# Optimization experiments

Hardware: AMD Instinct MI355X
Metric: run time of the kernel (lower is better)

Reference implementation:

```python
import jax, jax.numpy as jnp
import numpy as np

TOP_K = 2
NUM_EXPERTS = 8
ROUTE_SCALE = 1.0


def setup_inputs() -> dict:
    key = jax.random.key(0)
    ks = jax.random.split(key, 8)
    bs, slen, dim, hidden, E = 4, 1024, 2048, 1024, NUM_EXPERTS
    s = 0.02
    return {
        "x": jax.random.normal(ks[0], (bs, slen, dim), jnp.float32),
        "gate_w": jax.random.normal(ks[1], (E, dim), jnp.float32) * s,
        "w1": jax.random.normal(ks[2], (E, hidden, dim), jnp.float32) * s,
        "w2": jax.random.normal(ks[3], (E, dim, hidden), jnp.float32) * s,
        "w3": jax.random.normal(ks[4], (E, hidden, dim), jnp.float32) * s,
        "ws1": jax.random.normal(ks[5], (hidden, dim), jnp.float32) * s,
        "ws2": jax.random.normal(ks[6], (dim, hidden), jnp.float32) * s,
        "ws3": jax.random.normal(ks[7], (hidden, dim), jnp.float32) * s,
    }


def reference(x, gate_w, w1, w2, w3, ws1, ws2, ws3):
    bs, slen, dim = x.shape
    xf = x.reshape(-1, dim)  # (T, dim)
    # --- router: sigmoid scores in fp32, top-k (expert_bias is zeros at init) ---
    logits = (xf @ gate_w.T).astype(jnp.float32)  # (T, E)
    scores = jax.nn.sigmoid(logits)
    top_scores, sel_idx = jax.lax.top_k(scores, TOP_K)  # (T, k), (T, k)
    top_scores = top_scores * ROUTE_SCALE  # route_norm=False
    # --- routed experts: score_before_experts=True -> scale input by score ---
    routed = jnp.zeros_like(xf)
    for k in range(TOP_K):
        xs = xf * top_scores[:, k][:, None]  # (T, dim)
        h1 = jnp.einsum('td,ehd->teh', xs, w1)
        h3 = jnp.einsum('td,ehd->teh', xs, w3)
        h = jax.nn.silu(h1) * h3  # (T, E, hidden)
        onehot = jax.nn.one_hot(sel_idx[:, k], NUM_EXPERTS, dtype=h.dtype)  # (T, E)
        routed = routed + jnp.einsum('teh,te,edh->td', h, onehot, w2)
    # --- shared expert (SwiGLU FFN) ---
    shared = (jax.nn.silu(xf @ ws1.T) * (xf @ ws3.T)) @ ws2.T
    out = (shared + routed).reshape(bs, slen, dim)
    return out
```

## Files before the change

### kernel.cpp

```cpp
#include <hip/hip_runtime.h>
#include <hip/hip_bf16.h>
#include <cstdint>

#define TTOK   4096
#define DIM    2048
#define HID    1024
#define NEXP   8
#define GROWS  12288

typedef __attribute__((ext_vector_type(8))) __bf16 bf16x8;
typedef __attribute__((ext_vector_type(4))) float  f32x4;

__device__ __forceinline__ void glds16(const void* g, void* l) {
  __builtin_amdgcn_global_load_lds((const __attribute__((address_space(1))) void*)g,
                                   (__attribute__((address_space(3))) void*)l,
                                   16, 0, 0);
}

#define BAR() do { asm volatile("" ::: "memory"); __builtin_amdgcn_s_barrier(); \
                   asm volatile("" ::: "memory"); } while (0)

__global__ void convert_router_k(const float* __restrict__ w1, const float* __restrict__ w2,
                                 const float* __restrict__ w3, const float* __restrict__ ws1,
                                 const float* __restrict__ ws2, const float* __restrict__ ws3,
                                 __bf16* __restrict__ w13, __bf16* __restrict__ w2c,
                                 const float* __restrict__ x, const float* __restrict__ gw,
                                 int* __restrict__ sel, float* __restrict__ sco,
                                 int* __restrict__ counts) {
  const int N1 = 9 * 2048 * 2048 / 8;
  const int N2 = 9 * 2048 * 1024 / 8;
  const int CONV_BLOCKS = (N1 + N2) / 256;

  if (blockIdx.x < (unsigned)CONV_BLOCKS) {
    int s = blockIdx.x * 256 + threadIdx.x;
    const float* src;
    __bf16* dst;
    if (s < N1) {
      int e  = s / 524288;
      int r  = (s % 524288) / 256;
      int c  = (s % 256) * 8;
      int nr;
      if (r < 1024) { src = (e < 8 ? w1 + ((size_t)e * 1024 + r) * 2048 : ws1 + (size_t)r * 2048) + c;
                      nr = 2 * r; }
      else          { src = (e < 8 ? w3 + ((size_t)e * 1024 + (r - 1024)) * 2048 : ws3 + (size_t)(r - 1024) * 2048) + c;
                      nr = 2 * (r - 1024) + 1; }
      dst = w13 + ((size_t)e * 2048 + nr) * 2048 + c;
    } else {
      int s2 = s - N1;
      int e  = s2 / 262144;
      int r  = (s2 % 262144) / 128;
      int c  = (s2 % 128) * 8;
      src = (e < 8 ? w2 + ((size_t)e * 2048 + r) * 1024 : ws2 + (size_t)r * 1024) + c;
      dst = w2c + ((size_t)e * 2048 + r) * 1024 + c;
    }
    float4 a = *(const float4*)(src);
    float4 b = *(const float4*)(src + 4);
    bf16x8 o;
    o[0]=(__bf16)a.x; o[1]=(__bf16)a.y; o[2]=(__bf16)a.z; o[3]=(__bf16)a.w;
    o[4]=(__bf16)b.x; o[5]=(__bf16)b.y; o[6]=(__bf16)b.z; o[7]=(__bf16)b.w;
    *(bf16x8*)dst = o;
    return;
  }

  int t    = (blockIdx.x - CONV_BLOCKS) * 4 + (threadIdx.x >> 6);
  int lane = threadIdx.x & 63;
  const float* xr = x + (size_t)t * DIM;
  float acc[NEXP];
  #pragma unroll
  for (int e = 0; e < NEXP; ++e) acc[e] = 0.f;
  for (int d = lane * 4; d < DIM; d += 256) {
    float4 xv = *(const float4*)(xr + d);
    #pragma unroll
    for (int e = 0; e < NEXP; ++e) {
      float4 gv = *(const float4*)(gw + (size_t)e * DIM + d);
      acc[e] += xv.x * gv.x + xv.y * gv.y + xv.z * gv.z + xv.w * gv.w;
    }
  }
  #pragma unroll
  for (int off = 32; off; off >>= 1)
    #pragma unroll
    for (int e = 0; e < NEXP; ++e) acc[e] += __shfl_xor(acc[e], off);
  if (lane == 0) {
    float s[NEXP];
    #pragma unroll
    for (int e = 0; e < NEXP; ++e) s[e] = 1.f / (1.f + expf(-acc[e]));
    int e0 = 0;
    #pragma unroll
    for (int e = 1; e < NEXP; ++e) if (s[e] > s[e0]) e0 = e;
    int e1 = (e0 == 0) ? 1 : 0;
    #pragma unroll
    for (int e = 0; e < NEXP; ++e) if (e != e0 && s[e] > s[e1]) e1 = e;
    sel[2 * t] = e0; sel[2 * t + 1] = e1;
    sco[2 * t] = s[e0]; sco[2 * t + 1] = s[e1];
    atomicAdd(&counts[e0], 1); atomicAdd(&counts[e1], 1);
  }
}

__global__ void scan_k(const int* __restrict__ counts, int* __restrict__ offs) {
  if (threadIdx.x == 0 && blockIdx.x == 0) {
    int o = 0;
    for (int e = 0; e < NEXP; ++e) { offs[e] = o; o += counts[e]; }
    offs[NEXP] = o;
    offs[NEXP + 1] = o + TTOK;
  }
}

__global__ void gather_k(const float* __restrict__ x, const int* __restrict__ sel,
                         const float* __restrict__ sco, const int* __restrict__ offs,
                         int* __restrict__ cursor, int* __restrict__ token_rows,
                         __bf16* __restrict__ xg) {
  __shared__ int   rows[3];
  __shared__ float ss[3];
  int t = blockIdx.x;
  if (threadIdx.x == 0) {
    int e0 = sel[2 * t], e1 = sel[2 * t + 1];
    int r0 = offs[e0] + atomicAdd(&cursor[e0], 1);
    int r1 = offs[e1] + atomicAdd(&cursor[e1], 1);
    int r2 = 8192 + t;
    rows[0] = r0; rows[1] = r1; rows[2] = r2;
    ss[0] = sco[2 * t]; ss[1] = sco[2 * t + 1]; ss[2] = 1.0f;
    token_rows[3 * t] = r0; token_rows[3 * t + 1] = r1; token_rows[3 * t + 2] = r2;
  }
  __syncthreads();
  int c = threadIdx.x * 8;
  float4 v0 = *(const float4*)(x + (size_t)t * DIM + c);
  float4 v1 = *(const float4*)(x + (size_t)t * DIM + c + 4);
  #pragma unroll
  for (int j = 0; j < 3; ++j) {
    float s = ss[j];
    bf16x8 o;
    o[0]=(__bf16)(v0.x*s); o[1]=(__bf16)(v0.y*s); o[2]=(__bf16)(v0.z*s); o[3]=(__bf16)(v0.w*s);
    o[4]=(__bf16)(v1.x*s); o[5]=(__bf16)(v1.y*s); o[6]=(__bf16)(v1.z*s); o[7]=(__bf16)(v1.w*s);
    *(bf16x8*)(xg + (size_t)rows[j] * DIM + c) = o;
  }
}

template <int EPI>
__launch_bounds__(256)
__global__ void gemm_nt(const __bf16* __restrict__ A, const __bf16* __restrict__ Bw,
                        __bf16* __restrict__ Hb, float* __restrict__ c2a, float* __restrict__ c2b,
                        const int* __restrict__ offs, int K_, int N_) {
  int z  = blockIdx.z;
  int o0 = offs[z];
  int ne = offs[z + 1] - o0;

  int flat = blockIdx.y * 32 + blockIdx.x;
  int xcd  = flat & 7;
  int r    = flat >> 3;
  int s    = r >> 4;
  int pos  = r & 15;
  int bm   = ((xcd >> 2) + 2 * s) * 4 + (pos & 3);
  int bn   = (xcd & 3) * 4 + (pos >> 2);

  if (bm * 128 >= ne) return;

  const __bf16* Aseg = A  + (size_t)(o0 + bm * 128) * K_;
  const __bf16* Bseg = Bw + ((size_t)z * N_ + bn * 128) * K_;

  __shared__ __align__(16) __bf16 sA[2][128 * 64];
  __shared__ __align__(16) __bf16 sB[2][128 * 64];

  int tid  = threadIdx.x;
  int wave = tid >> 6, lane = tid & 63;
  int wm = wave & 1, wn = wave >> 1;
  int fr = lane & 15;
  int fq = lane >> 4;
  int sw = fr & 7;

  f32x4 acc[4][4];
  #pragma unroll
  for (int i = 0; i < 4; ++i)
    #pragma unroll
    for (int j = 0; j < 4; ++j) acc[i][j] = (f32x4){0.f, 0.f, 0.f, 0.f};

#define STAGE(buf, kbase)                                                     \
  {                                                                           \
    _Pragma("unroll")                                                         \
    for (int it = 0; it < 4; ++it) {                                          \
      int ss_ = it * 256 + tid;                                               \
      int row = ss_ >> 3;                                                     \
      int c8  = (ss_ & 7) ^ (row & 7);                                        \
      glds16(Aseg + (size_t)row * K_ + (kbase) + c8 * 8, &sA[buf][ss_ * 8]);  \
      glds16(Bseg + (size_t)row * K_ + (kbase) + c8 * 8, &sB[buf][ss_ * 8]);  \
    }                                                                         \
  }

  STAGE(0, 0)
  asm volatile("s_waitcnt vmcnt(0)" ::: "memory");
  BAR();

  const int nk = K_ >> 6;
  for (int t = 0; t < nk; ++t) {
    int cur = t & 1;
    if (t + 1 < nk) {
      STAGE(cur ^ 1, (t + 1) << 6)
      asm volatile("s_waitcnt vmcnt(8)" ::: "memory");
    } else {
      asm volatile("s_waitcnt vmcnt(0)" ::: "memory");
    }
    BAR();

    const __bf16* rAbase = &sA[cur][(wm * 64 + fr) * 64];
    const __bf16* rBbase = &sB[cur][(wn * 64 + fr) * 64];
    #pragma unroll
    for (int kk = 0; kk < 2; ++kk) {
      int slot = ((kk * 4 + fq) ^ sw) * 8;
      bf16x8 af[4], bb[4];
      #pragma unroll
      for (int i = 0; i < 4; ++i) af[i] = *(const bf16x8*)(rAbase + i * 16 * 64 + slot);
      #pragma unroll
      for (int i = 0; i < 4; ++i) bb[i] = *(const bf16x8*)(rBbase + i * 16 * 64 + slot);
      #pragma unroll
      for (int mi = 0; mi < 4; ++mi)
        #pragma unroll
        for (int ni = 0; ni < 4; ++ni)
          acc[mi][ni] = __builtin_amdgcn_mfma_f32_16x16x32_bf16(af[mi], bb[ni], acc[mi][ni], 0, 0, 0);
    }
    BAR();
  }
#undef STAGE

  #pragma unroll
  for (int mi = 0; mi < 4; ++mi) {
    #pragma unroll
    for (int rr = 0; rr < 4; ++rr) {
      int rl = bm * 128 + wm * 64 + mi * 16 + fq * 4 + rr;
      bool ok = rl < ne;
      int grow = o0 + rl;
      if (EPI == 0) {
        #pragma unroll
        for (int ni = 0; ni < 4; ++ni) {
          float v = acc[mi][ni][rr];
          float o = __shfl_xor(v, 1);
          float h1 = (fr & 1) ? o : v;
          float h3 = (fr & 1) ? v : o;
          float g  = h1 / (1.f + expf(-h1)) * h3;
          if (ok && !(fr & 1)) {
            int hcol = bn * 64 + wn * 32 + ni * 8 + (fr >> 1);
            Hb[(size_t)grow * 1024 + hcol] = (__bf16)g;
          }
        }
      } else {
        if (ok) {
          float* dst = (grow < 8192) ? (c2a + (size_t)grow * 2048)
                                     : (c2b + (size_t)(grow - 8192) * 2048);
          #pragma unroll
          for (int ni = 0; ni < 4; ++ni) {
            int col = bn * 128 + wn * 64 + ni * 16 + fr;
            dst[col] = acc[mi][ni][rr];
          }
        }
      }
    }
  }
}

__global__ void combine_k(const float* __restrict__ c2a, const float* __restrict__ c2b,
                          const int* __restrict__ token_rows, float* __restrict__ out) {
  __shared__ int rr[3];
  int t = blockIdx.x;
  if (threadIdx.x < 3) rr[threadIdx.x] = token_rows[3 * t + threadIdx.x];
  __syncthreads();
  int c = threadIdx.x * 8;
  const float* p0 = c2a + (size_t)rr[0] * 2048 + c;
  const float* p1 = c2a + (size_t)rr[1] * 2048 + c;
  const float* p2 = c2b + (size_t)(rr[2] - 8192) * 2048 + c;
  float4 a0 = *(const float4*)p0,       a1 = *(const float4*)p1,       a2 = *(const float4*)p2;
  float4 b0 = *(const float4*)(p0 + 4), b1 = *(const float4*)(p1 + 4), b2 = *(const float4*)(p2 + 4);
  float4 oa, ob;
  oa.x = a0.x + a1.x + a2.x; oa.y = a0.y + a1.y + a2.y;
  oa.z = a0.z + a1.z + a2.z; oa.w = a0.w + a1.w + a2.w;
  ob.x = b0.x + b1.x + b2.x; ob.y = b0.y + b1.y + b2.y;
  ob.z = b0.z + b1.z + b2.z; ob.w = b0.w + b1.w + b2.w;
  float* op = out + (size_t)t * 2048 + c;
  *(float4*)op = oa;
  *(float4*)(op + 4) = ob;
}

extern "C" void kernel_launch(void* const* d_in, const int* in_sizes, int n_in,
                              void* d_out, int out_size, void* d_ws, size_t ws_size,
                              hipStream_t stream) {
  const float* x   = (const float*)d_in[0];
  const float* gw  = (const float*)d_in[1];
  const float* w1  = (const float*)d_in[2];
  const float* w2  = (const float*)d_in[3];
  const float* w3  = (const float*)d_in[4];
  const float* ws1 = (const float*)d_in[5];
  const float* ws2 = (const float*)d_in[6];
  const float* ws3 = (const float*)d_in[7];
  float* out = (float*)d_out;

  char* p = (char*)d_ws;
  int*   counts     = (int*)p;
  int*   cursor     = (int*)(p + 64);
  int*   offs       = (int*)(p + 128);
  int*   sel        = (int*)(p + 1024);
  float* sco        = (float*)(p + 1024 + 32768);
  int*   token_rows = (int*)(p + 1024 + 65536);
  char* big = p + (1 << 20);
  __bf16* w13  = (__bf16*)big;
  __bf16* w2c  = (__bf16*)(big + 75497472ull);
  __bf16* xg   = (__bf16*)(big + 75497472ull + 37748736ull);
  __bf16* hbuf = (__bf16*)(big + 75497472ull + 37748736ull + 50331648ull);
  float*  c2a  = (float*)w13;
  float*  c2b  = (float*)xg;

  hipMemsetAsync(p, 0, 256, stream);

  convert_router_k<<<27648 + TTOK / 4, 256, 0, stream>>>(w1, w2, w3, ws1, ws2, ws3, w13, w2c,
                                                         x, gw, sel, sco, counts);
  scan_k<<<1, 64, 0, stream>>>(counts, offs);
  gather_k<<<TTOK, 256, 0, stream>>>(x, sel, sco, offs, cursor, token_rows, xg);
  gemm_nt<0><<<dim3(32, 16, 9), 256, 0, stream>>>(xg, w13, hbuf, nullptr, nullptr, offs, 2048, 2048);
  gemm_nt<1><<<dim3(32, 16, 9), 256, 0, stream>>>(hbuf, w2c, nullptr, c2a, c2b, offs, 1024, 2048);
  combine_k<<<TTOK, 256, 0, stream>>>(c2a, c2b, token_rows, out);
}
```

Baseline: 717.3 us.

## Grid-stride weight conversion with wider per-thread work and fused last-block scan

```diff
diff --git a/kernel.cpp b/kernel.cpp
--- a/kernel.cpp
+++ b/kernel.cpp
@@ -26,39 +26,49 @@
                                  __bf16* __restrict__ w13, __bf16* __restrict__ w2c,
                                  const float* __restrict__ x, const float* __restrict__ gw,
                                  int* __restrict__ sel, float* __restrict__ sco,
-                                 int* __restrict__ counts) {
-  const int N1 = 9 * 2048 * 2048 / 8;
-  const int N2 = 9 * 2048 * 1024 / 8;
-  const int CONV_BLOCKS = (N1 + N2) / 256;
+                                 int* __restrict__ counts, int* __restrict__ done,
+                                 int* __restrict__ offs) {
+  const int N1  = 9 * 2048 * 2048 / 8;
+  const int NP1 = N1 / 2;
+  const int NP2 = 9 * 2048 * 1024 / 16;
+  const int CONV_BLOCKS = 2048;
 
   if (blockIdx.x < (unsigned)CONV_BLOCKS) {
-    int s = blockIdx.x * 256 + threadIdx.x;
-    const float* src;
-    __bf16* dst;
-    if (s < N1) {
-      int e  = s / 524288;
-      int r  = (s % 524288) / 256;
-      int c  = (s % 256) * 8;
-      int nr;
-      if (r < 1024) { src = (e < 8 ? w1 + ((size_t)e * 1024 + r) * 2048 : ws1 + (size_t)r * 2048) + c;
-                      nr = 2 * r; }
-      else          { src = (e < 8 ? w3 + ((size_t)e * 1024 + (r - 1024)) * 2048 : ws3 + (size_t)(r - 1024) * 2048) + c;
-                      nr = 2 * (r - 1024) + 1; }
-      dst = w13 + ((size_t)e * 2048 + nr) * 2048 + c;
-    } else {
-      int s2 = s - N1;
-      int e  = s2 / 262144;
-      int r  = (s2 % 262144) / 128;
-      int c  = (s2 % 128) * 8;
-      src = (e < 8 ? w2 + ((size_t)e * 2048 + r) * 1024 : ws2 + (size_t)r * 1024) + c;
-      dst = w2c + ((size_t)e * 2048 + r) * 1024 + c;
-    }
-    float4 a = *(const float4*)(src);
-    float4 b = *(const float4*)(src + 4);
-    bf16x8 o;
-    o[0]=(__bf16)a.x; o[1]=(__bf16)a.y; o[2]=(__bf16)a.z; o[3]=(__bf16)a.w;
-    o[4]=(__bf16)b.x; o[5]=(__bf16)b.y; o[6]=(__bf16)b.z; o[7]=(__bf16)b.w;
-    *(bf16x8*)dst = o;
+    for (int pcur = blockIdx.x * 256 + threadIdx.x; pcur < NP1 + NP2;
+         pcur += CONV_BLOCKS * 256) {
+      const float* src;
+      __bf16* dst;
+      if (pcur < NP1) {
+        int s = 2 * pcur;
+        int e = s / 524288;
+        int r = (s % 524288) / 256;
+        int c = (s % 256) * 8;
+        int nr;
+        if (r < 1024) { src = (e < 8 ? w1 + ((size_t)e * 1024 + r) * 2048 : ws1 + (size_t)r * 2048) + c;
+                        nr = 2 * r; }
+        else          { src = (e < 8 ? w3 + ((size_t)e * 1024 + (r - 1024)) * 2048 : ws3 + (size_t)(r - 1024) * 2048) + c;
+                        nr = 2 * (r - 1024) + 1; }
+        dst = w13 + ((size_t)e * 2048 + nr) * 2048 + c;
+      } else {
+        int s2 = 2 * (pcur - NP1);
+        int e  = s2 / 262144;
+        int r  = (s2 % 262144) / 128;
+        int c  = (s2 % 128) * 8;
+        src = (e < 8 ? w2 + ((size_t)e * 2048 + r) * 1024 : ws2 + (size_t)r * 1024) + c;
+        dst = w2c + ((size_t)e * 2048 + r) * 1024 + c;
+      }
+      float4 a = *(const float4*)(src);
+      float4 b = *(const float4*)(src + 4);
+      float4 c4 = *(const float4*)(src + 8);
+      float4 d4 = *(const float4*)(src + 12);
+      bf16x8 o1, o2;
+      o1[0]=(__bf16)a.x;  o1[1]=(__bf16)a.y;  o1[2]=(__bf16)a.z;  o1[3]=(__bf16)a.w;
+      o1[4]=(__bf16)b.x;  o1[5]=(__bf16)b.y;  o1[6]=(__bf16)b.z;  o1[7]=(__bf16)b.w;
+      o2[0]=(__bf16)c4.x; o2[1]=(__bf16)c4.y; o2[2]=(__bf16)c4.z; o2[3]=(__bf16)c4.w;
+      o2[4]=(__bf16)d4.x; o2[5]=(__bf16)d4.y; o2[6]=(__bf16)d4.z; o2[7]=(__bf16)d4.w;
+      *(bf16x8*)dst = o1;
+      *(bf16x8*)(dst + 8) = o2;
+    }
     return;
   }
 
@@ -94,14 +104,20 @@
     sco[2 * t] = s[e0]; sco[2 * t + 1] = s[e1];
     atomicAdd(&counts[e0], 1); atomicAdd(&counts[e1], 1);
   }
-}
-
-__global__ void scan_k(const int* __restrict__ counts, int* __restrict__ offs) {
-  if (threadIdx.x == 0 && blockIdx.x == 0) {
-    int o = 0;
-    for (int e = 0; e < NEXP; ++e) { offs[e] = o; o += counts[e]; }
-    offs[NEXP] = o;
-    offs[NEXP + 1] = o + TTOK;
+  __syncthreads();
+  if (threadIdx.x == 0) {
+    __threadfence();
+    int old = atomicAdd(done, 1);
+    if (old == 1023) {
+      int o = 0;
+      #pragma unroll
+      for (int e = 0; e < NEXP; ++e) {
+        int c = atomicAdd(&counts[e], 0);
+        offs[e] = o; o += c;
+      }
+      offs[NEXP] = o;
+      offs[NEXP + 1] = o + TTOK;
+    }
   }
 }
 
@@ -294,6 +310,7 @@
   int*   counts     = (int*)p;
   int*   cursor     = (int*)(p + 64);
   int*   offs       = (int*)(p + 128);
+  int*   done       = (int*)(p + 192);
   int*   sel        = (int*)(p + 1024);
   float* sco        = (float*)(p + 1024 + 32768);
   int*   token_rows = (int*)(p + 1024 + 65536);
@@ -307,9 +324,8 @@
 
   hipMemsetAsync(p, 0, 256, stream);
 
-  convert_router_k<<<27648 + TTOK / 4, 256, 0, stream>>>(w1, w2, w3, ws1, ws2, ws3, w13, w2c,
-                                                         x, gw, sel, sco, counts);
-  scan_k<<<1, 64, 0, stream>>>(counts, offs);
+  convert_router_k<<<3072, 256, 0, stream>>>(w1, w2, w3, ws1, ws2, ws3, w13, w2c,
+                                             x, gw, sel, sco, counts, done, offs);
   gather_k<<<TTOK, 256, 0, stream>>>(x, sel, sco, offs, cursor, token_rows, xg);
   gemm_nt<0><<<dim3(32, 16, 9), 256, 0, stream>>>(xg, w13, hbuf, nullptr, nullptr, offs, 2048, 2048);
   gemm_nt<1><<<dim3(32, 16, 9), 256, 0, stream>>>(hbuf, w2c, nullptr, c2a, c2b, offs, 1024, 2048);
```

Result: no change. 725.6 us (+1.2%).
